# Kernel tuning notes

Hardware: AMD Instinct MI355X
Metric: run time of the kernel (lower is better)

Reference implementation:

```python
import jax, jax.numpy as jnp
import numpy as np
from jax import lax

H = 192; W = 192; C = 256; N = H * W; E = 294912; K = 289; DSIG = 1
SLOPE = 0.01
EPS = 1e-5


def leaky(x):
    return jnp.where(x >= 0, x, SLOPE * x)


def conv2d(x, w, pad, groups):
    return lax.conv_general_dilated(
        x, w, (1, 1), [(pad, pad), (pad, pad)],
        dimension_numbers=('NCHW', 'OIHW', 'NCHW'),
        feature_group_count=groups)


def bn2d(x, g, b):
    # BatchNorm2d with track_running_stats=False -> always batch stats (biased var)
    m = x.mean(axis=(0, 2, 3), keepdims=True)
    v = x.var(axis=(0, 2, 3), keepdims=True)
    return (x - m) / jnp.sqrt(v + EPS) * g.reshape(1, -1, 1, 1) + b.reshape(1, -1, 1, 1)


def conv_batch(x, w, g, b, pad, groups):
    # nn.Sequential(LeakyReLU(0.01), Conv2d(bias=False), BatchNorm2d)
    return bn2d(conv2d(leaky(x), w, pad, groups), g, b)


def bn1d(x, g, b):
    m = x.mean(axis=0)
    v = x.var(axis=0)
    return (x - m) / jnp.sqrt(v + EPS) * g + b


def setup_inputs() -> dict:
    key = jax.random.key(0)
    ks = jax.random.split(key, 20)
    X = jax.random.normal(ks[0], (N, C), dtype=jnp.float32)
    src = jax.random.randint(ks[1], (E,), 0, N)
    dst = jax.random.randint(ks[2], (E,), 0, N)
    k1 = jax.random.randint(ks[3], (E,), 0, K)
    k2 = jax.random.randint(ks[4], (E,), 0, K)
    InfoIdx = jnp.stack([src, k1, dst, k2], axis=1).astype(jnp.int64)
    edgmsk = (jax.random.uniform(ks[5], (E, 1)) < 0.9).astype(jnp.float32)
    s = 0.05
    inp = {
        'X': X, 'InfoIdx': InfoIdx, 'edgmsk': edgmsk,
        # PPM: depthwise 17x17 conv_batch then 1x1 conv_batch
        'ppm_w0': jax.random.normal(ks[6], (C, 1, 17, 17), jnp.float32) * s,
        'ppm_g0': jnp.ones((C,), jnp.float32), 'ppm_b0': jnp.zeros((C,), jnp.float32),
        'ppm_w1': jax.random.normal(ks[7], (C, C, 1, 1), jnp.float32) * s,
        'ppm_g1': jnp.ones((C,), jnp.float32), 'ppm_b1': jnp.zeros((C,), jnp.float32),
        # FFN_1: two 1x1 conv_batch
        'ffn1_w0': jax.random.normal(ks[8], (C, C, 1, 1), jnp.float32) * s,
        'ffn1_g0': jnp.ones((C,), jnp.float32), 'ffn1_b0': jnp.zeros((C,), jnp.float32),
        'ffn1_w1': jax.random.normal(ks[9], (C, C, 1, 1), jnp.float32) * s,
        'ffn1_g1': jnp.ones((C,), jnp.float32), 'ffn1_b1': jnp.zeros((C,), jnp.float32),
        # Dis: Linear(C,C) -> LeakyReLU -> Linear(C, 289)
        'dis_w1': jax.random.normal(ks[10], (C, C), jnp.float32) * s,
        'dis_b1': jnp.zeros((C,), jnp.float32),
        'dis_w2': jax.random.normal(ks[11], (K * DSIG, C), jnp.float32) * s,
        'dis_b2': jnp.zeros((K * DSIG,), jnp.float32),
        # BatchNorm1d
        'bn_g': jnp.ones((C,), jnp.float32), 'bn_b': jnp.zeros((C,), jnp.float32),
        # FFN_2 = DoubleConv: depthwise-expand 3x3 (groups=C, out=4C) then 1x1
        'ffn2_w0': jax.random.normal(ks[12], (4 * C, 1, 3, 3), jnp.float32) * s,
        'ffn2_g0': jnp.ones((4 * C,), jnp.float32), 'ffn2_b0': jnp.zeros((4 * C,), jnp.float32),
        'ffn2_w1': jax.random.normal(ks[13], (C, 4 * C, 1, 1), jnp.float32) * s,
        'ffn2_g1': jnp.ones((C,), jnp.float32), 'ffn2_b1': jnp.zeros((C,), jnp.float32),
    }
    return inp


def reference(X, InfoIdx, edgmsk,
              ppm_w0, ppm_g0, ppm_b0, ppm_w1, ppm_g1, ppm_b1,
              ffn1_w0, ffn1_g0, ffn1_b0, ffn1_w1, ffn1_g1, ffn1_b1,
              dis_w1, dis_b1, dis_w2, dis_b2, bn_g, bn_b,
              ffn2_w0, ffn2_g0, ffn2_b0, ffn2_w1, ffn2_g1, ffn2_b1):
    src_idx = InfoIdx[:, 0]
    dst_idx = InfoIdx[:, 2]
    # [N,C] -> [1,C,H,W]
    img = X.T.reshape(1, C, H, W)
    # PPM residual
    t = conv_batch(img, ppm_w0, ppm_g0, ppm_b0, pad=8, groups=C)
    t = conv_batch(t, ppm_w1, ppm_g1, ppm_b1, pad=0, groups=1)
    img = img + t
    # FFN_1 residual
    t = conv_batch(img, ffn1_w0, ffn1_g0, ffn1_b0, pad=0, groups=1)
    t = conv_batch(t, ffn1_w1, ffn1_g1, ffn1_b1, pad=0, groups=1)
    img = img + t
    Xn = img.reshape(C, N).T  # [N, C]
    # Dis MLP -> signal [N, 289, d_signal]
    h = leaky(Xn @ dis_w1.T + dis_b1)
    signal = (h @ dis_w2.T + dis_b2).reshape(N, K, DSIG)
    # edge gather + exp/clamp score
    s_src = signal[src_idx, InfoIdx[:, 1]]  # [E, 1]
    s_dst = signal[dst_idx, InfoIdx[:, 3]]  # [E, 1]
    aij = jnp.exp(jnp.clip(s_src + s_dst, -5.0, 5.0)) * edgmsk  # [E, 1]
    # two scatter-sum reductions to dst nodes
    A_sum = jax.ops.segment_sum(aij, dst_idx, num_segments=N)  # [N, 1]
    XA_sum = jax.ops.segment_sum(Xn[src_idx] * aij, dst_idx, num_segments=N)  # [N, C]
    X_trans = XA_sum / (A_sum + 1e-5)
    Xn = Xn + bn1d(X_trans, bn_g, bn_b)
    # FFN_2 = DoubleConv with residual skip
    img = Xn.T.reshape(1, C, H, W)
    t = conv_batch(img, ffn2_w0, ffn2_g0, ffn2_b0, pad=1, groups=C)
    t = conv_batch(t, ffn2_w1, ffn2_g1, ffn2_b1, pad=0, groups=1)
    out = t + img
    return out.reshape(C, N).T  # final bg.ndata['X'], [N, C]
```

## Files before the change

kernel.cpp:

```cpp
#include <hip/hip_runtime.h>
#include <cstddef>

#define HW 192
#define NP 36864
#define CH 256
#define EDGES 294912
#define KSIG 289
#define SLOPE 0.01f
#define BNEPS 1e-5f

typedef unsigned short u16;
typedef __attribute__((ext_vector_type(8))) short bf16x8;
typedef __attribute__((ext_vector_type(4))) float f32x4;

__device__ __forceinline__ float leaky(float x) { return x >= 0.f ? x : SLOPE * x; }
__device__ __forceinline__ u16 f2bf(float x) {
  unsigned u = __float_as_uint(x);
  unsigned r = (u + 0x7fffu + ((u >> 16) & 1u)) >> 16;
  return (u16)r;
}
__device__ __forceinline__ float bf2f(unsigned h) { return __uint_as_float(h << 16); }
__device__ __forceinline__ void bnss(const float* sums, const float* sqs,
                                     const float* g, const float* b, int k,
                                     float& s, float& h) {
  float mean = sums[k] * (1.f / NP);
  float var = sqs[k] * (1.f / NP) - mean * mean;
  s = g[k] * rsqrtf(var + BNEPS);
  h = b[k] - mean * s;
}

__global__ __launch_bounds__(256) void k_transpose(const float* __restrict__ src,
                                                   float* __restrict__ dst, int R, int S) {
  __shared__ float tile[32][33];
  int s0 = blockIdx.x * 32, r0 = blockIdx.y * 32;
  int tx = threadIdx.x & 31, ty = threadIdx.x >> 5;
#pragma unroll
  for (int j = 0; j < 4; j++) {
    int r = r0 + ty + 8 * j;
    tile[ty + 8 * j][tx] = src[(size_t)r * S + s0 + tx];
  }
  __syncthreads();
#pragma unroll
  for (int j = 0; j < 4; j++) {
    int s = s0 + ty + 8 * j;
    dst[(size_t)s * R + r0 + tx] = tile[tx][ty + 8 * j];
  }
}

__global__ __launch_bounds__(256) void k_cvtW(const float* __restrict__ pw1,
                                              const float* __restrict__ f1w0,
                                              const float* __restrict__ f1w1,
                                              const float* __restrict__ dw1,
                                              const float* __restrict__ dw2,
                                              const float* __restrict__ f2w1,
                                              u16* __restrict__ out) {
  int i = blockIdx.x * 256 + threadIdx.x;
  float v;
  if (i < 65536) v = pw1[i];
  else if (i < 131072) v = f1w0[i - 65536];
  else if (i < 196608) v = f1w1[i - 131072];
  else if (i < 262144) v = dw1[i - 196608];
  else if (i < 360448) { int j = i - 262144; v = (j < KSIG * 256) ? dw2[j] : 0.f; }
  else v = f2w1[i - 360448];
  out[i] = f2bf(v);
}

__global__ __launch_bounds__(256) void k_stats_f32(const float* __restrict__ Xr,
                                                   float* __restrict__ sums,
                                                   float* __restrict__ sqs) {
  int row = blockIdx.x;
  int t = threadIdx.x;
  const float4* p = (const float4*)(Xr + (size_t)row * NP);
  float s = 0.f, q = 0.f;
  for (int i = t; i < NP / 4; i += 256) {
    float4 v = p[i];
    s += v.x + v.y + v.z + v.w;
    q += v.x * v.x + v.y * v.y + v.z * v.z + v.w * v.w;
  }
  __shared__ float ss[256], qq[256];
  ss[t] = s; qq[t] = q;
  __syncthreads();
  for (int d = 128; d > 0; d >>= 1) {
    if (t < d) { ss[t] += ss[t + d]; qq[t] += qq[t + d]; }
    __syncthreads();
  }
  if (t == 0) { sums[row] = ss[0]; sqs[row] = qq[0]; }
}

__global__ __launch_bounds__(256) void k_stats_bf(const u16* __restrict__ Xr,
                                                  float* __restrict__ sums,
                                                  float* __restrict__ sqs) {
  int row = blockIdx.x;
  int t = threadIdx.x;
  const uint4* p = (const uint4*)(Xr + (size_t)row * NP);
  float s = 0.f, q = 0.f;
  for (int i = t; i < NP / 8; i += 256) {
    uint4 v = p[i];
    unsigned w[4] = {v.x, v.y, v.z, v.w};
#pragma unroll
    for (int j = 0; j < 4; j++) {
      float a = bf2f(w[j] & 0xffffu), c = bf2f(w[j] >> 16);
      s += a + c; q += a * a + c * c;
    }
  }
  __shared__ float ss[256], qq[256];
  ss[t] = s; qq[t] = q;
  __syncthreads();
  for (int d = 128; d > 0; d >>= 1) {
    if (t < d) { ss[t] += ss[t + d]; qq[t] += qq[t + d]; }
    __syncthreads();
  }
  if (t == 0) { sums[row] = ss[0]; sqs[row] = qq[0]; }
}

__global__ __launch_bounds__(256) void k_cvtT(const float* __restrict__ in,
                                              u16* __restrict__ outT, int M) {
  __shared__ float tile[32][65];
  int n0 = blockIdx.x * 64, k0 = blockIdx.y * 32;
  int t = threadIdx.x;
#pragma unroll
  for (int i = 0; i < 2; i++) {
    int ci = i * 256 + t;
    int k = ci >> 4, cg = (ci & 15) * 4;
    float4 v = *(const float4*)&in[(size_t)(k0 + k) * NP + n0 + cg];
    tile[k][cg] = v.x; tile[k][cg + 1] = v.y; tile[k][cg + 2] = v.z; tile[k][cg + 3] = v.w;
  }
  __syncthreads();
  int n = t >> 2, kg = (t & 3) * 8;
  uint4 o;
  o.x = (unsigned)f2bf(tile[kg + 0][n]) | ((unsigned)f2bf(tile[kg + 1][n]) << 16);
  o.y = (unsigned)f2bf(tile[kg + 2][n]) | ((unsigned)f2bf(tile[kg + 3][n]) << 16);
  o.z = (unsigned)f2bf(tile[kg + 4][n]) | ((unsigned)f2bf(tile[kg + 5][n]) << 16);
  o.w = (unsigned)f2bf(tile[kg + 6][n]) | ((unsigned)f2bf(tile[kg + 7][n]) << 16);
  *(uint4*)&outT[(size_t)(n0 + n) * M + k0 + kg] = o;
}

__global__ __launch_bounds__(256) void k_cvtTs(const float* __restrict__ in,
                                               u16* __restrict__ outT,
                                               const float* __restrict__ sums,
                                               const float* __restrict__ sqs,
                                               const float* __restrict__ g,
                                               const float* __restrict__ b, int M) {
  __shared__ float tile[32][65];
  int n0 = blockIdx.x * 64, k0 = blockIdx.y * 32;
  int t = threadIdx.x;
#pragma unroll
  for (int i = 0; i < 2; i++) {
    int ci = i * 256 + t;
    int k = ci >> 4, cg = (ci & 15) * 4;
    float s, h; bnss(sums, sqs, g, b, k0 + k, s, h);
    float4 v = *(const float4*)&in[(size_t)(k0 + k) * NP + n0 + cg];
    tile[k][cg]     = leaky(fmaf(v.x, s, h));
    tile[k][cg + 1] = leaky(fmaf(v.y, s, h));
    tile[k][cg + 2] = leaky(fmaf(v.z, s, h));
    tile[k][cg + 3] = leaky(fmaf(v.w, s, h));
  }
  __syncthreads();
  int n = t >> 2, kg = (t & 3) * 8;
  uint4 o;
  o.x = (unsigned)f2bf(tile[kg + 0][n]) | ((unsigned)f2bf(tile[kg + 1][n]) << 16);
  o.y = (unsigned)f2bf(tile[kg + 2][n]) | ((unsigned)f2bf(tile[kg + 3][n]) << 16);
  o.z = (unsigned)f2bf(tile[kg + 4][n]) | ((unsigned)f2bf(tile[kg + 5][n]) << 16);
  o.w = (unsigned)f2bf(tile[kg + 6][n]) | ((unsigned)f2bf(tile[kg + 7][n]) << 16);
  *(uint4*)&outT[(size_t)(n0 + n) * M + k0 + kg] = o;
}

__global__ __launch_bounds__(256) void k_cvtT_bf(const u16* __restrict__ in,
                                                 u16* __restrict__ outT,
                                                 const float* __restrict__ sums,
                                                 const float* __restrict__ sqs,
                                                 const float* __restrict__ g,
                                                 const float* __restrict__ b, int M) {
  __shared__ float tile[32][65];
  int n0 = blockIdx.x * 64, k0 = blockIdx.y * 32;
  int t = threadIdx.x;
  int k = t >> 3, cg = (t & 7) * 8;
  float s, h; bnss(sums, sqs, g, b, k0 + k, s, h);
  uint4 v = *(const uint4*)&in[(size_t)(k0 + k) * NP + n0 + cg];
  unsigned w[4] = {v.x, v.y, v.z, v.w};
#pragma unroll
  for (int j = 0; j < 4; j++) {
    tile[k][cg + 2 * j]     = leaky(fmaf(bf2f(w[j] & 0xffffu), s, h));
    tile[k][cg + 2 * j + 1] = leaky(fmaf(bf2f(w[j] >> 16), s, h));
  }
  __syncthreads();
  int n = t >> 2, kg = (t & 3) * 8;
  uint4 o;
  o.x = (unsigned)f2bf(tile[kg + 0][n]) | ((unsigned)f2bf(tile[kg + 1][n]) << 16);
  o.y = (unsigned)f2bf(tile[kg + 2][n]) | ((unsigned)f2bf(tile[kg + 3][n]) << 16);
  o.z = (unsigned)f2bf(tile[kg + 4][n]) | ((unsigned)f2bf(tile[kg + 5][n]) << 16);
  o.w = (unsigned)f2bf(tile[kg + 6][n]) | ((unsigned)f2bf(tile[kg + 7][n]) << 16);
  *(uint4*)&outT[(size_t)(n0 + n) * M + k0 + kg] = o;
}

__global__ __launch_bounds__(256) void k_fuse1(const float* __restrict__ base,
                                               const float* __restrict__ raw,
                                               const float* __restrict__ sums,
                                               const float* __restrict__ sqs,
                                               const float* __restrict__ g,
                                               const float* __restrict__ b,
                                               float* __restrict__ img2,
                                               u16* __restrict__ outT) {
  __shared__ float tile[32][65];
  int n0 = blockIdx.x * 64, k0 = blockIdx.y * 32;
  int t = threadIdx.x;
#pragma unroll
  for (int i = 0; i < 2; i++) {
    int ci = i * 256 + t;
    int k = ci >> 4, cg = (ci & 15) * 4;
    float s, h; bnss(sums, sqs, g, b, k0 + k, s, h);
    size_t idx = (size_t)(k0 + k) * NP + n0 + cg;
    float4 bv = *(const float4*)&base[idx];
    float4 rv = *(const float4*)&raw[idx];
    float4 o;
    o.x = bv.x + fmaf(rv.x, s, h); o.y = bv.y + fmaf(rv.y, s, h);
    o.z = bv.z + fmaf(rv.z, s, h); o.w = bv.w + fmaf(rv.w, s, h);
    *(float4*)&img2[idx] = o;
    tile[k][cg]     = leaky(o.x);
    tile[k][cg + 1] = leaky(o.y);
    tile[k][cg + 2] = leaky(o.z);
    tile[k][cg + 3] = leaky(o.w);
  }
  __syncthreads();
  int n = t >> 2, kg = (t & 3) * 8;
  uint4 o;
  o.x = (unsigned)f2bf(tile[kg + 0][n]) | ((unsigned)f2bf(tile[kg + 1][n]) << 16);
  o.y = (unsigned)f2bf(tile[kg + 2][n]) | ((unsigned)f2bf(tile[kg + 3][n]) << 16);
  o.z = (unsigned)f2bf(tile[kg + 4][n]) | ((unsigned)f2bf(tile[kg + 5][n]) << 16);
  o.w = (unsigned)f2bf(tile[kg + 6][n]) | ((unsigned)f2bf(tile[kg + 7][n]) << 16);
  *(uint4*)&outT[(size_t)(n0 + n) * CH + k0 + kg] = o;
}

__global__ __launch_bounds__(256) void k_fuse2(const float* __restrict__ base,
                                               const float* __restrict__ raw,
                                               const float* __restrict__ sums,
                                               const float* __restrict__ sqs,
                                               const float* __restrict__ g,
                                               const float* __restrict__ b,
                                               float* __restrict__ XnT,
                                               u16* __restrict__ outT) {
  __shared__ float tile[32][65];
  int n0 = blockIdx.x * 64, k0 = blockIdx.y * 32;
  int t = threadIdx.x;
#pragma unroll
  for (int i = 0; i < 2; i++) {
    int ci = i * 256 + t;
    int k = ci >> 4, cg = (ci & 15) * 4;
    float s, h; bnss(sums, sqs, g, b, k0 + k, s, h);
    size_t idx = (size_t)(k0 + k) * NP + n0 + cg;
    float4 bv = *(const float4*)&base[idx];
    float4 rv = *(const float4*)&raw[idx];
    tile[k][cg]     = bv.x + fmaf(rv.x, s, h);
    tile[k][cg + 1] = bv.y + fmaf(rv.y, s, h);
    tile[k][cg + 2] = bv.z + fmaf(rv.z, s, h);
    tile[k][cg + 3] = bv.w + fmaf(rv.w, s, h);
  }
  __syncthreads();
  int n = t >> 2, kg = (t & 3) * 8;
  float4 f0 = {tile[kg + 0][n], tile[kg + 1][n], tile[kg + 2][n], tile[kg + 3][n]};
  float4 f1 = {tile[kg + 4][n], tile[kg + 5][n], tile[kg + 6][n], tile[kg + 7][n]};
  *(float4*)&XnT[(size_t)(n0 + n) * CH + k0 + kg] = f0;
  *(float4*)&XnT[(size_t)(n0 + n) * CH + k0 + kg + 4] = f1;
  uint4 o;
  o.x = (unsigned)f2bf(f0.x) | ((unsigned)f2bf(f0.y) << 16);
  o.y = (unsigned)f2bf(f0.z) | ((unsigned)f2bf(f0.w) << 16);
  o.z = (unsigned)f2bf(f1.x) | ((unsigned)f2bf(f1.y) << 16);
  o.w = (unsigned)f2bf(f1.z) | ((unsigned)f2bf(f1.w) << 16);
  *(uint4*)&outT[(size_t)(n0 + n) * CH + k0 + kg] = o;
}

__global__ __launch_bounds__(256) void k_mgemm(const u16* __restrict__ A,
                                               const u16* __restrict__ Bt,
                                               float* __restrict__ Out,
                                               const float* __restrict__ bias,
                                               int K, int Mstore, int actout) {
  __shared__ u16 As[128 * 32];
  __shared__ u16 Bs[128 * 32];
  int t = threadIdx.x;
  int lane = t & 63, wave = t >> 6;
  int wm = (wave >> 1) * 64, wn = (wave & 1) * 64;
  int m0 = blockIdx.y * 128, n0 = blockIdx.x * 128;
  int r = lane & 15, q = lane >> 4;
  f32x4 acc[4][4];
#pragma unroll
  for (int a = 0; a < 4; a++)
#pragma unroll
    for (int b = 0; b < 4; b++) acc[a][b] = (f32x4){0.f, 0.f, 0.f, 0.f};

  for (int k0 = 0; k0 < K; k0 += 32) {
#pragma unroll
    for (int i = 0; i < 2; i++) {
      int cc = t + i * 256;
      int mm = cc >> 2, kq = (cc & 3) * 8;
      uint4 av = *(const uint4*)&A[(size_t)(m0 + mm) * K + k0 + kq];
      uint4 bv = *(const uint4*)&Bt[(size_t)(n0 + mm) * K + k0 + kq];
      *(uint4*)&As[mm * 32 + kq] = av;
      *(uint4*)&Bs[mm * 32 + kq] = bv;
    }
    __syncthreads();
    bf16x8 af[4], bfr[4];
#pragma unroll
    for (int mt = 0; mt < 4; mt++)
      af[mt] = *(const bf16x8*)&As[(wm + mt * 16 + r) * 32 + q * 8];
#pragma unroll
    for (int nt = 0; nt < 4; nt++)
      bfr[nt] = *(const bf16x8*)&Bs[(wn + nt * 16 + r) * 32 + q * 8];
#pragma unroll
    for (int mt = 0; mt < 4; mt++)
#pragma unroll
      for (int nt = 0; nt < 4; nt++)
        acc[mt][nt] = __builtin_amdgcn_mfma_f32_16x16x32_bf16(af[mt], bfr[nt], acc[mt][nt], 0, 0, 0);
    __syncthreads();
  }
#pragma unroll
  for (int mt = 0; mt < 4; mt++) {
    int mrow = m0 + wm + mt * 16 + q * 4;
#pragma unroll
    for (int i = 0; i < 4; i++) {
      int m = mrow + i;
      if (m >= Mstore) continue;
      float bs = bias ? bias[m] : 0.f;
#pragma unroll
      for (int nt = 0; nt < 4; nt++) {
        float v = acc[mt][nt][i] + bs;
        if (actout) v = leaky(v);
        Out[(size_t)m * NP + n0 + wn + nt * 16 + r] = v;
      }
    }
  }
}

__global__ __launch_bounds__(256) void k_dwconv17(const float* __restrict__ in,
                                                  const float* __restrict__ w,
                                                  float* __restrict__ out) {
  int c = blockIdx.y;
  int tile = blockIdx.x;
  int ty0 = (tile / 3) * 64, tx0 = (tile % 3) * 64;
  __shared__ __align__(16) float sm[80 * 84];
  const float* inc = in + (size_t)c * NP;
  for (int i = threadIdx.x; i < 80 * 80; i += 256) {
    int r = i / 80, cc = i - r * 80;
    int gy = ty0 + r - 8, gx = tx0 + cc - 8;
    float v = 0.f;
    if (gy >= 0 && gy < HW && gx >= 0 && gx < HW) v = leaky(inc[gy * HW + gx]);
    sm[r * 84 + cc] = v;
  }
  __syncthreads();
  int tr = threadIdx.x >> 4, tc = threadIdx.x & 15;
  float acc[4][4];
#pragma unroll
  for (int oy = 0; oy < 4; oy++)
#pragma unroll
    for (int j = 0; j < 4; j++) acc[oy][j] = 0.f;
  const float* wc = w + c * 289;
  for (int iy = 0; iy < 20; iy++) {
    const float* rowp = &sm[(4 * tr + iy) * 84 + 4 * tc];
    float win[20];
#pragma unroll
    for (int i = 0; i < 5; i++) {
      float4 v = *(const float4*)(rowp + 4 * i);
      win[4 * i] = v.x; win[4 * i + 1] = v.y; win[4 * i + 2] = v.z; win[4 * i + 3] = v.w;
    }
    int lo = iy - 16; if (lo < 0) lo = 0;
    int hi = iy; if (hi > 3) hi = 3;
#pragma unroll
    for (int oy = 0; oy < 4; oy++) {
      if (oy < lo || oy > hi) continue;
      const float* wr = wc + (iy - oy) * 17;
#pragma unroll
      for (int kx = 0; kx < 17; kx++) {
        float wv = wr[kx];
        acc[oy][0] = fmaf(wv, win[kx + 0], acc[oy][0]);
        acc[oy][1] = fmaf(wv, win[kx + 1], acc[oy][1]);
        acc[oy][2] = fmaf(wv, win[kx + 2], acc[oy][2]);
        acc[oy][3] = fmaf(wv, win[kx + 3], acc[oy][3]);
      }
    }
  }
#pragma unroll
  for (int oy = 0; oy < 4; oy++) {
    float4 o = {acc[oy][0], acc[oy][1], acc[oy][2], acc[oy][3]};
    *(float4*)(out + (size_t)c * NP + (ty0 + 4 * tr + oy) * HW + tx0 + 4 * tc) = o;
  }
}

__global__ __launch_bounds__(256) void k_conv3x4(const float* __restrict__ in,
                                                 const float* __restrict__ w,
                                                 u16* __restrict__ out) {
  int wave = threadIdx.x >> 6, lane = threadIdx.x & 63;
  int c = blockIdx.y;
  int y = blockIdx.x * 4 + wave;
  const float* wc = w + (size_t)(4 * c) * 9;
  float wr[36];
#pragma unroll
  for (int k = 0; k < 36; k++) wr[k] = wc[k];
  float acc[4][3];
#pragma unroll
  for (int oc = 0; oc < 4; oc++)
#pragma unroll
    for (int s = 0; s < 3; s++) acc[oc][s] = 0.f;
  const float* base = in + (size_t)c * NP;
#pragma unroll
  for (int ky = 0; ky < 3; ky++) {
    int ry = y + ky - 1;
    if (ry < 0 || ry >= HW) continue;
    const float* rp = base + ry * HW;
    float a0 = leaky(rp[lane]);
    float a1 = leaky(rp[64 + lane]);
    float a2 = leaky(rp[128 + lane]);
    float e0 = __shfl(a0, 63), e1 = __shfl(a1, 63);
    float b1 = __shfl(a1, 0),  b2 = __shfl(a2, 0);
    float l0 = __shfl_up(a0, 1); if (lane == 0) l0 = 0.f;
    float l1 = __shfl_up(a1, 1); if (lane == 0) l1 = e0;
    float l2 = __shfl_up(a2, 1); if (lane == 0) l2 = e1;
    float r0 = __shfl_down(a0, 1); if (lane == 63) r0 = b1;
    float r1 = __shfl_down(a1, 1); if (lane == 63) r1 = b2;
    float r2 = __shfl_down(a2, 1); if (lane == 63) r2 = 0.f;
#pragma unroll
    for (int oc = 0; oc < 4; oc++) {
      float w0 = wr[oc * 9 + ky * 3], w1 = wr[oc * 9 + ky * 3 + 1], w2 = wr[oc * 9 + ky * 3 + 2];
      acc[oc][0] = fmaf(w0, l0, fmaf(w1, a0, fmaf(w2, r0, acc[oc][0])));
      acc[oc][1] = fmaf(w0, l1, fmaf(w1, a1, fmaf(w2, r1, acc[oc][1])));
      acc[oc][2] = fmaf(w0, l2, fmaf(w1, a2, fmaf(w2, r2, acc[oc][2])));
    }
  }
  size_t ob = (size_t)(4 * c) * NP + (size_t)y * HW + lane;
#pragma unroll
  for (int oc = 0; oc < 4; oc++) {
    out[ob + (size_t)oc * NP]       = f2bf(acc[oc][0]);
    out[ob + (size_t)oc * NP + 64]  = f2bf(acc[oc][1]);
    out[ob + (size_t)oc * NP + 128] = f2bf(acc[oc][2]);
  }
}

__global__ __launch_bounds__(256) void k_edge(const int* __restrict__ info,
                                              const float* __restrict__ msk,
                                              const float* __restrict__ sig,
                                              float* __restrict__ aij,
                                              int* __restrict__ counts) {
  int e = blockIdx.x * 256 + threadIdx.x;
  int4 ii = ((const int4*)info)[e];
  float s = sig[(size_t)ii.y * NP + ii.x] + sig[(size_t)ii.w * NP + ii.z];
  s = fminf(fmaxf(s, -5.f), 5.f);
  aij[e] = expf(s) * msk[e];
  atomicAdd(&counts[ii.z], 1);
}

__global__ __launch_bounds__(256) void k_scan1(const int* __restrict__ counts,
                                               int* __restrict__ offsets,
                                               int* __restrict__ bsum) {
  __shared__ int sm[256];
  int t = threadIdx.x;
  int i = blockIdx.x * 256 + t;
  int v = counts[i];
  sm[t] = v;
  __syncthreads();
  for (int d = 1; d < 256; d <<= 1) {
    int add = (t >= d) ? sm[t - d] : 0;
    __syncthreads();
    sm[t] += add;
    __syncthreads();
  }
  offsets[i] = sm[t] - v;
  if (t == 255) bsum[blockIdx.x] = sm[255];
}
__global__ __launch_bounds__(256) void k_scan2(const int* __restrict__ bsum,
                                               int* __restrict__ boff) {
  __shared__ int sm[256];
  int t = threadIdx.x;
  int v = (t < 144) ? bsum[t] : 0;
  sm[t] = v;
  __syncthreads();
  for (int d = 1; d < 256; d <<= 1) {
    int add = (t >= d) ? sm[t - d] : 0;
    __syncthreads();
    sm[t] += add;
    __syncthreads();
  }
  boff[t] = sm[t] - v;
}
__global__ __launch_bounds__(256) void k_scan3(int* __restrict__ offsets,
                                               const int* __restrict__ boff,
                                               int* __restrict__ cursor) {
  int i = blockIdx.x * 256 + threadIdx.x;
  int o = offsets[i] + boff[blockIdx.x];
  offsets[i] = o;
  cursor[i] = o;
  if (i == 0) offsets[NP] = EDGES;
}
__global__ __launch_bounds__(256) void k_scatter(const int* __restrict__ info,
                                                 int* __restrict__ cursor,
                                                 int* __restrict__ sorted) {
  int e = blockIdx.x * 256 + threadIdx.x;
  int d = info[4 * e + 2];
  int pos = atomicAdd(&cursor[d], 1);
  sorted[pos] = e;
}

__global__ __launch_bounds__(256) void k_agg(const int* __restrict__ offsets,
                                             const int* __restrict__ sorted,
                                             const float* __restrict__ aij,
                                             const int* __restrict__ info,
                                             const u16* __restrict__ XnBf,
                                             float* __restrict__ Xtr) {
  int wave = threadIdx.x >> 6, lane = threadIdx.x & 63;
  int node = blockIdx.x * 4 + wave;
  int o0 = offsets[node], o1 = offsets[node + 1];
  float ax = 0.f, ay = 0.f, az = 0.f, aw = 0.f, asum = 0.f;
  for (int i = o0; i < o1; i++) {
    int e = sorted[i];
    float a = aij[e];
    int s = info[4 * e];
    uint2 v = ((const uint2*)(XnBf + (size_t)s * CH))[lane];
    ax = fmaf(a, bf2f(v.x & 0xffffu), ax);
    ay = fmaf(a, bf2f(v.x >> 16), ay);
    az = fmaf(a, bf2f(v.y & 0xffffu), az);
    aw = fmaf(a, bf2f(v.y >> 16), aw);
    asum += a;
  }
  float inv = 1.f / (asum + 1e-5f);
  float4 o = {ax * inv, ay * inv, az * inv, aw * inv};
  ((float4*)(Xtr + (size_t)node * CH))[lane] = o;
}

__global__ __launch_bounds__(256) void k_colstats(const float* __restrict__ Xt,
                                                  float* __restrict__ sums,
                                                  float* __restrict__ sqs) {
  int c = threadIdx.x;
  float s = 0.f, q = 0.f;
  for (int n = blockIdx.x; n < NP; n += gridDim.x) {
    float v = Xt[(size_t)n * CH + c];
    s += v; q += v * v;
  }
  atomicAdd(&sums[c], s);
  atomicAdd(&sqs[c], q);
}

__global__ __launch_bounds__(256) void k_mkimg4(const float* __restrict__ Xn,
                                                const float* __restrict__ Xtr,
                                                const float* __restrict__ sums,
                                                const float* __restrict__ sqs,
                                                const float* __restrict__ g,
                                                const float* __restrict__ b,
                                                float* __restrict__ img4) {
  __shared__ float tile[32][33];
  int c0 = blockIdx.x * 32, n0 = blockIdx.y * 32;
  int tx = threadIdx.x & 31, ty = threadIdx.x >> 5;
  int c = c0 + tx;
  float s, h; bnss(sums, sqs, g, b, c, s, h);
#pragma unroll
  for (int j = 0; j < 4; j++) {
    size_t idx = (size_t)(n0 + ty + 8 * j) * CH + c;
    tile[ty + 8 * j][tx] = Xn[idx] + fmaf(Xtr[idx], s, h);
  }
  __syncthreads();
#pragma unroll
  for (int j = 0; j < 4; j++) {
    int cc = c0 + ty + 8 * j;
    img4[(size_t)cc * NP + n0 + tx] = tile[tx][ty + 8 * j];
  }
}

__global__ __launch_bounds__(256) void k_final(const float* __restrict__ raw5,
                                               const float* __restrict__ img4,
                                               const float* __restrict__ sums,
                                               const float* __restrict__ sqs,
                                               const float* __restrict__ g,
                                               const float* __restrict__ b,
                                               float* __restrict__ out) {
  __shared__ float tile[32][33];
  int n0 = blockIdx.x * 32, c0 = blockIdx.y * 32;
  int tx = threadIdx.x & 31, ty = threadIdx.x >> 5;
#pragma unroll
  for (int j = 0; j < 4; j++) {
    int c = c0 + ty + 8 * j;
    float s, h; bnss(sums, sqs, g, b, c, s, h);
    size_t idx = (size_t)c * NP + n0 + tx;
    tile[ty + 8 * j][tx] = fmaf(raw5[idx], s, h) + img4[idx];
  }
  __syncthreads();
#pragma unroll
  for (int j = 0; j < 4; j++) {
    int n = n0 + ty + 8 * j;
    out[(size_t)n * CH + c0 + tx] = tile[tx][ty + 8 * j];
  }
}

extern "C" void kernel_launch(void* const* d_in, const int* in_sizes, int n_in,
                              void* d_out, int out_size, void* d_ws, size_t ws_size,
                              hipStream_t stream) {
  (void)in_sizes; (void)n_in; (void)out_size; (void)ws_size;
  const float* X    = (const float*)d_in[0];
  const int*   info = (const int*)d_in[1];
  const float* msk  = (const float*)d_in[2];
  const float* pw0  = (const float*)d_in[3];
  const float* pg0  = (const float*)d_in[4];
  const float* pb0  = (const float*)d_in[5];
  const float* pw1  = (const float*)d_in[6];
  const float* pg1  = (const float*)d_in[7];
  const float* pb1  = (const float*)d_in[8];
  const float* f1w0 = (const float*)d_in[9];
  const float* f1g0 = (const float*)d_in[10];
  const float* f1b0 = (const float*)d_in[11];
  const float* f1w1 = (const float*)d_in[12];
  const float* f1g1 = (const float*)d_in[13];
  const float* f1b1 = (const float*)d_in[14];
  const float* dw1  = (const float*)d_in[15];
  const float* db1  = (const float*)d_in[16];
  const float* dw2  = (const float*)d_in[17];
  const float* db2  = (const float*)d_in[18];
  const float* bng  = (const float*)d_in[19];
  const float* bnb  = (const float*)d_in[20];
  const float* f2w0 = (const float*)d_in[21];
  const float* f2g0 = (const float*)d_in[22];
  const float* f2b0 = (const float*)d_in[23];
  const float* f2w1 = (const float*)d_in[24];
  const float* f2g1 = (const float*)d_in[25];
  const float* f2b1 = (const float*)d_in[26];
  float* out = (float*)d_out;

  float* ws = (float*)d_ws;
  float* sum0 = ws + 0;    float* sq0 = ws + 256;
  float* sum1 = ws + 512;  float* sq1 = ws + 768;
  float* sum2 = ws + 1024; float* sq2 = ws + 1280;
  float* sum3 = ws + 1536; float* sq3 = ws + 1792;
  float* sum5 = ws + 2048; float* sq5 = ws + 2304;
  float* sumT = ws + 2560; float* sqT = ws + 2816;
  float* sum4 = ws + 3072; float* sq4 = ws + 4096;
  int* counts  = (int*)(ws + 8192);
  int* offsets = (int*)(ws + 45056);
  int* cursor  = (int*)(ws + 82176);
  int* bsum    = (int*)(ws + 119296);
  int* boff    = (int*)(ws + 119552);
  int* sorted  = (int*)(ws + 131072);
  float* aij   = ws + 425984;
  const size_t S = (size_t)NP * CH;
  float* slotD = ws + 720896;
  float* slotB = slotD + S;
  float* slotA = slotB + S;
  float* slotC = slotA + S;
  u16* bfB  = (u16*)(slotC + S);
  u16* bfH  = bfB + S;
  float* sigT = (float*)(bfH + S);
  u16* bfW  = (u16*)(sigT + (size_t)KSIG * NP);
  u16* raw4bf  = (u16*)slotB;
  u16* bfT1024 = bfB;

  hipMemsetAsync(ws, 0, 5120 * sizeof(float), stream);
  hipMemsetAsync(counts, 0, NP * sizeof(int), stream);

  dim3 b256(256);
  k_cvtW<<<2432, b256, 0, stream>>>(pw1, f1w0, f1w1, dw1, dw2, f2w1, bfW);
  k_transpose<<<dim3(CH / 32, NP / 32), b256, 0, stream>>>(X, slotA, NP, CH);
  k_dwconv17<<<dim3(9, CH), b256, 0, stream>>>(slotA, pw0, slotB);
  k_stats_f32<<<CH, b256, 0, stream>>>(slotB, sum0, sq0);
  k_cvtTs<<<dim3(NP / 64, 8), b256, 0, stream>>>(slotB, bfB, sum0, sq0, pg0, pb0, CH);
  k_mgemm<<<dim3(NP / 128, 2), b256, 0, stream>>>(bfW, bfB, slotC, nullptr, CH, CH, 0);
  k_stats_f32<<<CH, b256, 0, stream>>>(slotC, sum1, sq1);
  k_fuse1<<<dim3(NP / 64, 8), b256, 0, stream>>>(slotA, slotC, sum1, sq1, pg1, pb1, slotD, bfB);
  k_mgemm<<<dim3(NP / 128, 2), b256, 0, stream>>>(bfW + 65536, bfB, slotB, nullptr, CH, CH, 0);
  k_stats_f32<<<CH, b256, 0, stream>>>(slotB, sum2, sq2);
  k_cvtTs<<<dim3(NP / 64, 8), b256, 0, stream>>>(slotB, bfB, sum2, sq2, f1g0, f1b0, CH);
  k_mgemm<<<dim3(NP / 128, 2), b256, 0, stream>>>(bfW + 131072, bfB, slotC, nullptr, CH, CH, 0);
  k_stats_f32<<<CH, b256, 0, stream>>>(slotC, sum3, sq3);
  k_fuse2<<<dim3(NP / 64, 8), b256, 0, stream>>>(slotD, slotC, sum3, sq3, f1g1, f1b1, slotA, bfB);
  k_mgemm<<<dim3(NP / 128, 2), b256, 0, stream>>>(bfW + 196608, bfB, slotC, db1, CH, CH, 1);
  k_cvtT<<<dim3(NP / 64, 8), b256, 0, stream>>>(slotC, bfH, CH);
  k_mgemm<<<dim3(NP / 128, 3), b256, 0, stream>>>(bfW + 262144, bfH, sigT, db2, CH, KSIG, 0);
  k_edge<<<EDGES / 256, b256, 0, stream>>>(info, msk, sigT, aij, counts);
  k_scan1<<<NP / 256, b256, 0, stream>>>(counts, offsets, bsum);
  k_scan2<<<1, b256, 0, stream>>>(bsum, boff);
  k_scan3<<<NP / 256, b256, 0, stream>>>(offsets, boff, cursor);
  k_scatter<<<EDGES / 256, b256, 0, stream>>>(info, cursor, sorted);
  k_agg<<<NP / 4, b256, 0, stream>>>(offsets, sorted, aij, info, bfB, slotD);
  k_colstats<<<288, b256, 0, stream>>>(slotD, sumT, sqT);
  k_mkimg4<<<dim3(CH / 32, NP / 32), b256, 0, stream>>>(slotA, slotD, sumT, sqT, bng, bnb, slotC);
  k_conv3x4<<<dim3(48, CH), b256, 0, stream>>>(slotC, f2w0, raw4bf);
  k_stats_bf<<<1024, b256, 0, stream>>>(raw4bf, sum4, sq4);
  k_cvtT_bf<<<dim3(NP / 64, 32), b256, 0, stream>>>(raw4bf, bfT1024, sum4, sq4, f2g0, f2b0, 1024);
  k_mgemm<<<dim3(NP / 128, 2), b256, 0, stream>>>(bfW + 360448, bfT1024, slotD, nullptr, 1024, CH, 0);
  k_stats_f32<<<CH, b256, 0, stream>>>(slotD, sum5, sq5);
  k_final<<<dim3(NP / 32, CH / 32), b256, 0, stream>>>(slotD, slotC, sum5, sq5, f2g1, f2b1, out);
}
```

Measured before the change: 737.0 us.

## Compute depthwise 17x17 conv with bf16 MFMA via Toeplitz weight matrix

```diff
diff --git a/kernel.cpp b/kernel.cpp
--- a/kernel.cpp
+++ b/kernel.cpp
@@ -336,51 +336,51 @@
   int c = blockIdx.y;
   int tile = blockIdx.x;
   int ty0 = (tile / 3) * 64, tx0 = (tile % 3) * 64;
-  __shared__ __align__(16) float sm[80 * 84];
+  __shared__ u16 smIn[80 * 88];
+  __shared__ u16 smT[17 * 16 * 40];
   const float* inc = in + (size_t)c * NP;
   for (int i = threadIdx.x; i < 80 * 80; i += 256) {
     int r = i / 80, cc = i - r * 80;
     int gy = ty0 + r - 8, gx = tx0 + cc - 8;
     float v = 0.f;
     if (gy >= 0 && gy < HW && gx >= 0 && gx < HW) v = leaky(inc[gy * HW + gx]);
-    sm[r * 84 + cc] = v;
-  }
-  __syncthreads();
-  int tr = threadIdx.x >> 4, tc = threadIdx.x & 15;
-  float acc[4][4];
-#pragma unroll
-  for (int oy = 0; oy < 4; oy++)
-#pragma unroll
-    for (int j = 0; j < 4; j++) acc[oy][j] = 0.f;
+    smIn[r * 88 + cc] = f2bf(v);
+  }
   const float* wc = w + c * 289;
-  for (int iy = 0; iy < 20; iy++) {
-    const float* rowp = &sm[(4 * tr + iy) * 84 + 4 * tc];
-    float win[20];
-#pragma unroll
-    for (int i = 0; i < 5; i++) {
-      float4 v = *(const float4*)(rowp + 4 * i);
-      win[4 * i] = v.x; win[4 * i + 1] = v.y; win[4 * i + 2] = v.z; win[4 * i + 3] = v.w;
+  for (int i = threadIdx.x; i < 17 * 16 * 32; i += 256) {
+    int ky = i >> 9;
+    int rem = i & 511;
+    int n = rem >> 5, kk = rem & 31;
+    int kx = kk - n;
+    float v = (kx >= 0 && kx < 17) ? wc[ky * 17 + kx] : 0.f;
+    smT[(ky * 16 + n) * 40 + kk] = f2bf(v);
+  }
+  __syncthreads();
+  int lane = threadIdx.x & 63, wave = threadIdx.x >> 6;
+  int wy = wave * 16;
+  int r = lane & 15, q = lane >> 4;
+  f32x4 acc[4];
+#pragma unroll
+  for (int xt = 0; xt < 4; xt++) acc[xt] = (f32x4){0.f, 0.f, 0.f, 0.f};
+#pragma unroll
+  for (int ky = 0; ky < 17; ky++) {
+    bf16x8 bfrag = *(const bf16x8*)&smT[(ky * 16 + r) * 40 + q * 8];
+    int rowA = wy + r + ky;
+#pragma unroll
+    for (int xt = 0; xt < 4; xt++) {
+      bf16x8 afrag = *(const bf16x8*)&smIn[rowA * 88 + xt * 16 + q * 8];
+      acc[xt] = __builtin_amdgcn_mfma_f32_16x16x32_bf16(afrag, bfrag, acc[xt], 0, 0, 0);
     }
-    int lo = iy - 16; if (lo < 0) lo = 0;
-    int hi = iy; if (hi > 3) hi = 3;
-#pragma unroll
-    for (int oy = 0; oy < 4; oy++) {
-      if (oy < lo || oy > hi) continue;
-      const float* wr = wc + (iy - oy) * 17;
-#pragma unroll
-      for (int kx = 0; kx < 17; kx++) {
-        float wv = wr[kx];
-        acc[oy][0] = fmaf(wv, win[kx + 0], acc[oy][0]);
-        acc[oy][1] = fmaf(wv, win[kx + 1], acc[oy][1]);
-        acc[oy][2] = fmaf(wv, win[kx + 2], acc[oy][2]);
-        acc[oy][3] = fmaf(wv, win[kx + 3], acc[oy][3]);
-      }
+  }
+  float* oc = out + (size_t)c * NP;
+#pragma unroll
+  for (int xt = 0; xt < 4; xt++) {
+    int x = tx0 + xt * 16 + r;
+#pragma unroll
+    for (int i = 0; i < 4; i++) {
+      int y = ty0 + wy + q * 4 + i;
+      oc[y * HW + x] = acc[xt][i];
     }
-  }
-#pragma unroll
-  for (int oy = 0; oy < 4; oy++) {
-    float4 o = {acc[oy][0], acc[oy][1], acc[oy][2], acc[oy][3]};
-    *(float4*)(out + (size_t)c * NP + (ty0 + 4 * tr + oy) * HW + tx0 + 4 * tc) = o;
   }
 }
 
```

Result: faster. 710.6 us (-3.6%).
